# Performance work log

Hardware: AMD Instinct MI355X
Metric: run time of the kernel (lower is better)

Reference implementation:

```python
import jax, jax.numpy as jnp
import numpy as np

B, H, W, C = 64, 56, 56, 192
NH, WS, SS = 6, 7, 3
N = WS * WS
MLP_H = 4 * C
HD = C // NH
NW = (H // WS) * (W // WS)
EPS = 1e-5


def _rel_pos_index():
    coords = np.stack(np.meshgrid(np.arange(WS), np.arange(WS), indexing='ij')).reshape(2, -1)
    rel = (coords[:, :, None] - coords[:, None, :]).transpose(1, 2, 0)
    rel[..., 0] += WS - 1
    rel[..., 1] += WS - 1
    rel[..., 0] *= 2 * WS - 1
    return rel.sum(-1)  # [N, N]


def _attn_mask():
    img = np.zeros((H, W))
    cnt = 0
    sl = (slice(0, -WS), slice(-WS, -SS), slice(-SS, None))
    for hs in sl:
        for ws in sl:
            img[hs, ws] = cnt
            cnt += 1
    mw = img.reshape(H // WS, WS, W // WS, WS).transpose(0, 2, 1, 3).reshape(-1, N)
    am = mw[:, None, :] - mw[:, :, None]
    return np.where(am != 0, -100.0, 0.0).astype(np.float32)  # [nW, N, N]


REL_IDX = jnp.asarray(_rel_pos_index())
ATTN_MASK = jnp.asarray(_attn_mask())


def _ln(x, g, b):
    m = x.mean(-1, keepdims=True)
    v = x.var(-1, keepdims=True)
    return (x - m) / jnp.sqrt(v + EPS) * g + b


def setup_inputs() -> dict:
    key = jax.random.key(0)
    ks = jax.random.split(key, 16)
    p = lambda k, shape: jax.random.normal(k, shape, dtype=jnp.float32) * 0.02
    return {
        'x': jax.random.normal(ks[0], (B, H * W, C), dtype=jnp.float32),
        'norm1_g': jnp.ones((C,), jnp.float32),
        'norm1_b': jnp.zeros((C,), jnp.float32),
        'qkv_w': p(ks[1], (3 * C, C)),
        'qkv_b': jnp.zeros((3 * C,), jnp.float32),
        'rpb': p(ks[2], ((2 * WS - 1) * (2 * WS - 1), NH)),
        'gate': jnp.full((NH,), 0.001, jnp.float32),
        'proj_w': p(ks[3], (C, C)),
        'proj_b': jnp.zeros((C,), jnp.float32),
        'norm2_g': jnp.ones((C,), jnp.float32),
        'norm2_b': jnp.zeros((C,), jnp.float32),
        'fc1_w': p(ks[4], (MLP_H, C)),
        'fc1_b': jnp.zeros((MLP_H,), jnp.float32),
        'bn_g': jnp.ones((MLP_H,), jnp.float32),
        'bn_b': jnp.zeros((MLP_H,), jnp.float32),
        'fc2_w': p(ks[5], (C, MLP_H)),
        'fc2_b': jnp.zeros((C,), jnp.float32),
    }


def reference(x, norm1_g, norm1_b, qkv_w, qkv_b, rpb, gate, proj_w, proj_b,
              norm2_g, norm2_b, fc1_w, fc1_b, bn_g, bn_b, fc2_w, fc2_b):
    shortcut = x  # [B, L, C]
    y = _ln(x, norm1_g, norm1_b).reshape(B, H, W, C)
    # cyclic shift
    y = jnp.roll(y, (-SS, -SS), axis=(1, 2))
    # window partition -> [B*nW, N, C]
    yw = y.reshape(B, H // WS, WS, W // WS, WS, C).transpose(0, 1, 3, 2, 4, 5).reshape(-1, N, C)
    qkv = (yw @ qkv_w.T + qkv_b).reshape(-1, N, 3, NH, HD).transpose(2, 0, 3, 1, 4)
    q, k, v = qkv[0], qkv[1], qkv[2]  # [B_, NH, N, HD]
    scale = HD ** (-0.5)
    attn = jnp.einsum('bhnd,bhmd->bhnm', q * scale, k)  # [B_, NH, N, N]
    bias = rpb[REL_IDX].transpose(2, 0, 1)  # [NH, N, N]
    attn = attn + bias[None]
    attn = attn.reshape(B, NW, NH, N, N) + ATTN_MASK[None, :, None]
    attn = jax.nn.softmax(attn.reshape(-1, NH, N, N), axis=-1)
    attn = attn * jax.nn.sigmoid(gate).reshape(1, NH, 1, 1)  # post-softmax gate
    o = jnp.einsum('bhnm,bhmd->bhnd', attn, v).transpose(0, 2, 1, 3).reshape(-1, N, C)
    o = o @ proj_w.T + proj_b
    # window reverse + reverse shift
    o = o.reshape(B, H // WS, W // WS, WS, WS, C).transpose(0, 1, 3, 2, 4, 5).reshape(B, H, W, C)
    o = jnp.roll(o, (SS, SS), axis=(1, 2)).reshape(B, H * W, C)
    x = shortcut + o
    # MLP with eval-mode BatchNorm1d (running_mean=0, running_var=1)
    z = _ln(x, norm2_g, norm2_b)
    z = z @ fc1_w.T + fc1_b
    z = z / jnp.sqrt(1.0 + EPS) * bn_g + bn_b
    z = jax.nn.gelu(z, approximate=False)
    z = z @ fc2_w.T + fc2_b
    return x + z
```

## Files before the change

### kernel.cpp

```cpp
#include <hip/hip_runtime.h>
#include <hip/hip_bf16.h>
#include <math.h>


typedef __attribute__((ext_vector_type(8))) short short8;
typedef __attribute__((ext_vector_type(4))) short short4v;
typedef __attribute__((ext_vector_type(4))) float floatx4;

static __device__ __forceinline__ float bf2f(__hip_bfloat16 v) { return __bfloat162float(v); }

static __device__ __forceinline__ short f2bs(float f) {
    union { __hip_bfloat16 h; short s; } u;
    u.h = __float2bfloat16(f);
    return u.s;
}

__global__ __launch_bounds__(256)
void cvt_w(const float* __restrict__ a, const float* __restrict__ b,
           const float* __restrict__ c, const float* __restrict__ d,
           __hip_bfloat16* __restrict__ o)
{
    int i = blockIdx.x * 256 + threadIdx.x;
    float v;
    if (i < 110592)      v = a[i];
    else if (i < 147456) v = b[i - 110592];
    else if (i < 294912) {
        int l = i - 147456;
        int j = l & 7, ln = (l >> 3) & 63, t = l >> 9;
        int ks = t % 6, cc = t / 6;
        v = c[(cc * 16 + (ln & 15)) * 192 + ks * 32 + (ln >> 4) * 8 + j];
    } else {
        int l = i - 294912;
        int j = l & 7, ln = (l >> 3) & 63, t = l >> 9;
        int kg = t % 24, cc = t / 24;
        v = d[(cc * 16 + (ln & 15)) * 768 + kg * 32 + (ln >> 4) * 8 + j];
    }
    o[i] = __float2bfloat16(v);
}

__global__ __launch_bounds__(256)
void ln1_shift_win(const float* __restrict__ x,
                   const float* __restrict__ g,
                   const float* __restrict__ bt,
                   __hip_bfloat16* __restrict__ yw)
{
    int r = blockIdx.x * 4 + (threadIdx.x >> 6);
    int lane = threadIdx.x & 63;
    int win = r / 49, t = r - win * 49;
    int b = win >> 6, wi = win & 63;
    int wh = wi >> 3, ww = wi & 7;
    int tr = t / 7, tc = t - tr * 7;
    int hs = wh * 7 + tr + 3; if (hs >= 56) hs -= 56;
    int ws = ww * 7 + tc + 3; if (ws >= 56) ws -= 56;
    const float* src = x + ((size_t)b * 3136 + hs * 56 + ws) * 192;
    float v0 = src[lane];
    float v1 = src[lane + 64];
    float v2 = src[lane + 128];
    float s  = v0 + v1 + v2;
    float s2 = v0 * v0 + v1 * v1 + v2 * v2;
#pragma unroll
    for (int off = 32; off; off >>= 1) { s += __shfl_xor(s, off); s2 += __shfl_xor(s2, off); }
    float mean = s * (1.0f / 192.0f);
    float var  = s2 * (1.0f / 192.0f) - mean * mean;
    float rstd = rsqrtf(var + 1e-5f);
    __hip_bfloat16* dst = yw + (size_t)r * 192;
    dst[lane]       = __float2bfloat16((v0 - mean) * rstd * g[lane]       + bt[lane]);
    dst[lane + 64]  = __float2bfloat16((v1 - mean) * rstd * g[lane + 64]  + bt[lane + 64]);
    dst[lane + 128] = __float2bfloat16((v2 - mean) * rstd * g[lane + 128] + bt[lane + 128]);
}

__global__ __launch_bounds__(256)
void build_tbl(const float* __restrict__ rpb, float* __restrict__ tbl)
{
    int bid = blockIdx.x;
    int head = bid >> 2, cls = bid & 3;
    int ch = cls >> 1, cw = cls & 1;
    for (int idx = threadIdx.x; idx < 4096; idx += 256) {
        int tile = idx >> 8, lane = (idx >> 2) & 63, rg = idx & 3;
        int mt = tile >> 2, nt = tile & 3;
        int lm = lane & 15, quad = lane >> 4;
        int i = nt * 16 + lm;
        int j = mt * 16 + quad * 4 + rg;
        float v;
        if (i >= 49 || j >= 49) {
            v = -1e30f;
        } else {
            int ri = i / 7, ci = i - ri * 7;
            int rj = j / 7, cj = j - rj * 7;
            int bidx = (ri - rj + 6) * 13 + (ci - cj + 6);
            v = rpb[bidx * 6 + head];
            int rio = ch ? (ri < 4 ? 1 : 2) : 0;
            int cio = cw ? (ci < 4 ? 1 : 2) : 0;
            int rjo = ch ? (rj < 4 ? 1 : 2) : 0;
            int cjo = cw ? (cj < 4 ? 1 : 2) : 0;
            if (rio * 3 + cio != rjo * 3 + cjo) v -= 100.0f;
        }
        tbl[(size_t)bid * 4096 + idx] = v;
    }
}

__global__ __launch_bounds__(256)
void attn_mfma(const __hip_bfloat16* __restrict__ qkv,
               const float* __restrict__ tbl,
               const float* __restrict__ gate,
               __hip_bfloat16* __restrict__ o)
{
    __shared__ __align__(16) char lds[49152];
    const int wave = threadIdx.x >> 6, lane = threadIdx.x & 63;
    const int lm = lane & 15, quad = lane >> 4;
    const int idx = blockIdx.x * 4 + wave;
    const int win = idx / 6;
    const int head = idx - win * 6;
    const int wi = win & 63;
    const int cls = (((wi >> 3) == 7) ? 2 : 0) + (((wi & 7) == 7) ? 1 : 0);

    char* vTb = lds + wave * 12288;
    char* Pb  = vTb + 4096;

    const __hip_bfloat16* base = qkv + (size_t)win * 49 * 576 + head * 32;

    {
        short8 v0 = {0,0,0,0,0,0,0,0}, v1 = {0,0,0,0,0,0,0,0};
        short8 v2 = {0,0,0,0,0,0,0,0}, v3 = {0,0,0,0,0,0,0,0};
        if (lane < 49) {
            const short* p = (const short*)(base + 384) + (size_t)lane * 576;
            v0 = *(const short8*)(p);
            v1 = *(const short8*)(p + 8);
            v2 = *(const short8*)(p + 16);
            v3 = *(const short8*)(p + 24);
        }
#pragma unroll
        for (int d = 0; d < 32; ++d) {
            short val = (d < 8) ? v0[d & 7] : (d < 16) ? v1[d & 7] : (d < 24) ? v2[d & 7] : v3[d & 7];
            *(short*)(vTb + ((d * 128 + lane * 2) ^ ((d & 7) << 4))) = val;
        }
    }

    short8 qf[4], kf[4];
    const short* qsrc = (const short*)base + quad * 8;
    const short* ksrc = (const short*)(base + 192) + quad * 8;
#pragma unroll
    for (int tt = 0; tt < 4; ++tt) {
        int t = tt * 16 + lm;
        if (t < 49) {
            qf[tt] = *(const short8*)(qsrc + (size_t)t * 576);
            kf[tt] = *(const short8*)(ksrc + (size_t)t * 576);
        } else {
            qf[tt] = (short8){0,0,0,0,0,0,0,0};
            kf[tt] = (short8){0,0,0,0,0,0,0,0};
        }
    }

    const floatx4 z4 = {0.f, 0.f, 0.f, 0.f};
    floatx4 s[4][4];
#pragma unroll
    for (int mt = 0; mt < 4; ++mt)
#pragma unroll
        for (int nt = 0; nt < 4; ++nt)
            s[mt][nt] = __builtin_amdgcn_mfma_f32_16x16x32_bf16(kf[mt], qf[nt], z4, 0, 0, 0);

    const float* tb = tbl + (size_t)(head * 4 + cls) * 4096 + lane * 4;
#pragma unroll
    for (int mt = 0; mt < 4; ++mt)
#pragma unroll
        for (int nt = 0; nt < 4; ++nt) {
            floatx4 b = *(const floatx4*)(tb + (mt * 4 + nt) * 256);
#pragma unroll
            for (int rg = 0; rg < 4; ++rg)
                s[mt][nt][rg] = s[mt][nt][rg] * 0.17677669529663689f + b[rg];
        }

    const float gt = 1.0f / (1.0f + __expf(-gate[head]));

    float inv[4];
#pragma unroll
    for (int nt = 0; nt < 4; ++nt) {
        float mx = -1e30f;
#pragma unroll
        for (int mt = 0; mt < 4; ++mt)
#pragma unroll
            for (int rg = 0; rg < 4; ++rg) mx = fmaxf(mx, s[mt][nt][rg]);
        mx = fmaxf(mx, __shfl_xor(mx, 16));
        mx = fmaxf(mx, __shfl_xor(mx, 32));
        float sum = 0.f;
#pragma unroll
        for (int mt = 0; mt < 4; ++mt)
#pragma unroll
            for (int rg = 0; rg < 4; ++rg) {
                float e = __expf(s[mt][nt][rg] - mx);
                s[mt][nt][rg] = e;
                sum += e;
            }
        sum += __shfl_xor(sum, 16);
        sum += __shfl_xor(sum, 32);
        inv[nt] = gt / sum;
    }

#pragma unroll
    for (int nt = 0; nt < 4; ++nt) {
        int row = nt * 16 + lm;
#pragma unroll
        for (int mt = 0; mt < 4; ++mt) {
            short4v pk = { f2bs(s[mt][nt][0] * inv[nt]), f2bs(s[mt][nt][1] * inv[nt]),
                           f2bs(s[mt][nt][2] * inv[nt]), f2bs(s[mt][nt][3] * inv[nt]) };
            int off = (row * 128 + mt * 32 + quad * 8) ^ ((row & 7) << 4);
            *(short4v*)(Pb + off) = pk;
        }
    }

    floatx4 oacc[4][2];
#pragma unroll
    for (int pt = 0; pt < 4; ++pt)
#pragma unroll
        for (int nt = 0; nt < 2; ++nt) oacc[pt][nt] = z4;

#pragma unroll
    for (int ks = 0; ks < 2; ++ks) {
        short8 vfr[2];
#pragma unroll
        for (int nt = 0; nt < 2; ++nt) {
            int row = nt * 16 + lm;
            vfr[nt] = *(const short8*)(vTb + ((row * 128 + ks * 64 + quad * 16) ^ ((row & 7) << 4)));
        }
#pragma unroll
        for (int pt = 0; pt < 4; ++pt) {
            int row = pt * 16 + lm;
            short8 pfr = *(const short8*)(Pb + ((row * 128 + ks * 64 + quad * 16) ^ ((row & 7) << 4)));
#pragma unroll
            for (int nt = 0; nt < 2; ++nt)
                oacc[pt][nt] = __builtin_amdgcn_mfma_f32_16x16x32_bf16(pfr, vfr[nt], oacc[pt][nt], 0, 0, 0);
        }
    }

    __hip_bfloat16* obase = o + (size_t)win * 49 * 192 + head * 32;
#pragma unroll
    for (int pt = 0; pt < 4; ++pt) {
#pragma unroll
        for (int rg = 0; rg < 4; ++rg) {
            int q = pt * 16 + quad * 4 + rg;
            if (q < 49) {
#pragma unroll
                for (int nt = 0; nt < 2; ++nt)
                    obase[(size_t)q * 192 + nt * 16 + lm] = __float2bfloat16(oacc[pt][nt][rg]);
            }
        }
    }
}

template <int MODE>
__global__ __launch_bounds__(256, 2)
void gemm_bt(const __hip_bfloat16* __restrict__ A,
             const __hip_bfloat16* __restrict__ W,
             const float* __restrict__ bias,
             const float* __restrict__ ex0,
             void* __restrict__ OutV,
             int K, int Ncols)
{
    __shared__ __align__(16) char lds[(128 * 32 + 64 * 32) * 2];
    short* sA = (short*)lds;
    short* sB = (short*)(lds + 8192);

    const int tid  = threadIdx.x;
    const int wave = tid >> 6, lane = tid & 63;
    const int m0 = blockIdx.x * 128;
    const int n0 = blockIdx.y * 64;
    const int wm = wave >> 1, wn = wave & 1;
    const int lm = lane & 15, quad = lane >> 4;

    floatx4 acc[4][2];
#pragma unroll
    for (int mt = 0; mt < 4; ++mt)
#pragma unroll
        for (int nt = 0; nt < 2; ++nt) acc[mt][nt] = (floatx4){0.f, 0.f, 0.f, 0.f};

    for (int kk = 0; kk < K; kk += 32) {
#pragma unroll
        for (int i = 0; i < 2; ++i) {
            int c = i * 256 + tid;
            int row = c >> 2, kc = c & 3;
            const __hip_bfloat16* gp = A + (size_t)(m0 + row) * K + kk + kc * 8;
            char* lp = lds + (i * 256 + wave * 64) * 16;
            __builtin_amdgcn_global_load_lds((const __attribute__((address_space(1))) void*)gp,
                                             (__attribute__((address_space(3))) void*)lp, 16, 0, 0);
        }
        {
            int c = tid;
            int row = c >> 2, kc = c & 3;
            const __hip_bfloat16* gp = W + (size_t)(n0 + row) * K + kk + kc * 8;
            char* lp = lds + 8192 + (wave * 64) * 16;
            __builtin_amdgcn_global_load_lds((const __attribute__((address_space(1))) void*)gp,
                                             (__attribute__((address_space(3))) void*)lp, 16, 0, 0);
        }
        asm volatile("s_waitcnt vmcnt(0)" ::: "memory");
        __syncthreads();

        short8 af[4], bf[2];
#pragma unroll
        for (int mt = 0; mt < 4; ++mt)
            af[mt] = *(const short8*)(sA + ((wm * 64 + mt * 16 + lm) * 32 + quad * 8));
#pragma unroll
        for (int nt = 0; nt < 2; ++nt)
            bf[nt] = *(const short8*)(sB + ((wn * 32 + nt * 16 + lm) * 32 + quad * 8));
#pragma unroll
        for (int mt = 0; mt < 4; ++mt)
#pragma unroll
            for (int nt = 0; nt < 2; ++nt)
                acc[mt][nt] = __builtin_amdgcn_mfma_f32_16x16x32_bf16(af[mt], bf[nt], acc[mt][nt], 0, 0, 0);
        __syncthreads();
    }

#pragma unroll
    for (int mt = 0; mt < 4; ++mt) {
#pragma unroll
        for (int nt = 0; nt < 2; ++nt) {
            int col = n0 + wn * 32 + nt * 16 + lm;
            float bcol = bias[col];
#pragma unroll
            for (int rg = 0; rg < 4; ++rg) {
                int row = m0 + wm * 64 + mt * 16 + quad * 4 + rg;
                float val = acc[mt][nt][rg] + bcol;
                if (MODE == 0) {
                    ((__hip_bfloat16*)OutV)[(size_t)row * Ncols + col] = __float2bfloat16(val);
                } else {
                    int win = row / 49, t = row - win * 49;
                    int b = win >> 6, wi = win & 63;
                    int wh = wi >> 3, ww = wi & 7;
                    int tr = t / 7, tc = t - tr * 7;
                    int h = wh * 7 + tr + 3; if (h >= 56) h -= 56;
                    int w = ww * 7 + tc + 3; if (w >= 56) w -= 56;
                    size_t dst = ((size_t)b * 3136 + h * 56 + w) * 192 + col;
                    ((float*)OutV)[dst] = val + ex0[dst];
                }
            }
        }
    }
}

__global__ __launch_bounds__(256, 2)
void mlp_fused(float* __restrict__ xio,
               const __hip_bfloat16* __restrict__ w1f,
               const __hip_bfloat16* __restrict__ w2f,
               const float* __restrict__ fc1_b,
               const float* __restrict__ bn_g,
               const float* __restrict__ bn_b,
               const float* __restrict__ fc2_b,
               const float* __restrict__ n2g,
               const float* __restrict__ n2b)
{
    __shared__ __align__(16) char zb[128 * 384];
    __shared__ __align__(16) char hbf[128 * 128];

    const int tid = threadIdx.x;
    const int wave = tid >> 6, lane = tid & 63;
    const int lm = lane & 15, quad = lane >> 4;
    const int wm = wave >> 1, wn = wave & 1;
    const int m0 = blockIdx.x * 128;

    {
        float g0 = n2g[lane], g1 = n2g[lane + 64], g2 = n2g[lane + 128];
        float b0 = n2b[lane], b1 = n2b[lane + 64], b2 = n2b[lane + 128];
        for (int rr = 0; rr < 32; ++rr) {
            int row = wave * 32 + rr;
            const float* src = xio + (size_t)(m0 + row) * 192;
            float v0 = src[lane], v1 = src[lane + 64], v2 = src[lane + 128];
            float s = v0 + v1 + v2;
            float s2 = v0 * v0 + v1 * v1 + v2 * v2;
#pragma unroll
            for (int off = 32; off; off >>= 1) { s += __shfl_xor(s, off); s2 += __shfl_xor(s2, off); }
            float mean = s * (1.0f / 192.0f);
            float var  = s2 * (1.0f / 192.0f) - mean * mean;
            float rstd = rsqrtf(var + 1e-5f);
            int rx = (row & 7) << 4;
            int rb = row * 384;
            *(short*)(zb + ((rb + lane * 2)       ^ rx)) = f2bs((v0 - mean) * rstd * g0 + b0);
            *(short*)(zb + ((rb + 128 + lane * 2) ^ rx)) = f2bs((v1 - mean) * rstd * g1 + b1);
            *(short*)(zb + ((rb + 256 + lane * 2) ^ rx)) = f2bs((v2 - mean) * rstd * g2 + b2);
        }
    }
    __syncthreads();

    floatx4 acc[4][6];
#pragma unroll
    for (int mt = 0; mt < 4; ++mt)
#pragma unroll
        for (int nt = 0; nt < 6; ++nt) acc[mt][nt] = (floatx4){0.f, 0.f, 0.f, 0.f};

    const short8* w1v = (const short8*)w1f;
    const short8* w2v = (const short8*)w2f;

    for (int s = 0; s < 12; ++s) {
        {
            floatx4 a2[4][2];
#pragma unroll
            for (int mt = 0; mt < 4; ++mt)
#pragma unroll
                for (int nt = 0; nt < 2; ++nt) a2[mt][nt] = (floatx4){0.f, 0.f, 0.f, 0.f};
            const int c0 = s * 4 + wn * 2;
#pragma unroll
            for (int ks = 0; ks < 6; ++ks) {
                short8 wf0 = w1v[(size_t)(c0 * 6 + ks) * 64 + lane];
                short8 wf1 = w1v[(size_t)((c0 + 1) * 6 + ks) * 64 + lane];
                short8 zf[4];
#pragma unroll
                for (int mt = 0; mt < 4; ++mt) {
                    int row = wm * 64 + mt * 16 + lm;
                    int byte = (row * 384 + ks * 64 + quad * 16) ^ ((row & 7) << 4);
                    zf[mt] = *(const short8*)(zb + byte);
                }
#pragma unroll
                for (int mt = 0; mt < 4; ++mt) {
                    a2[mt][0] = __builtin_amdgcn_mfma_f32_16x16x32_bf16(wf0, zf[mt], a2[mt][0], 0, 0, 0);
                    a2[mt][1] = __builtin_amdgcn_mfma_f32_16x16x32_bf16(wf1, zf[mt], a2[mt][1], 0, 0, 0);
                }
            }
#pragma unroll
            for (int nt = 0; nt < 2; ++nt) {
                int colb = (c0 + nt) * 16 + quad * 4;
                float fb[4], G[4], B2[4];
#pragma unroll
                for (int rg = 0; rg < 4; ++rg) {
                    fb[rg] = fc1_b[colb + rg];
                    G[rg]  = bn_g[colb + rg] * 0.99999500003749968f;
                    B2[rg] = bn_b[colb + rg];
                }
#pragma unroll
                for (int mt = 0; mt < 4; ++mt) {
                    int row = wm * 64 + mt * 16 + lm;
                    short4v pk;
#pragma unroll
                    for (int rg = 0; rg < 4; ++rg) {
                        float t2 = (a2[mt][nt][rg] + fb[rg]) * G[rg] + B2[rg];
                        float ge = 0.5f * t2 * (1.0f + erff(t2 * 0.70710678118654752f));
                        pk[rg] = f2bs(ge);
                    }
                    int byte = (row * 128 + (wn * 2 + nt) * 32 + quad * 8) ^ ((row & 7) << 4);
                    *(short4v*)(hbf + byte) = pk;
                }
            }
        }
        __syncthreads();
        {
#pragma unroll
            for (int ks = 0; ks < 2; ++ks) {
                const int kg = s * 2 + ks;
                short8 vf[6];
#pragma unroll
                for (int nt = 0; nt < 6; ++nt)
                    vf[nt] = w2v[(size_t)((wn * 6 + nt) * 24 + kg) * 64 + lane];
                short8 hf[4];
#pragma unroll
                for (int mt = 0; mt < 4; ++mt) {
                    int row = wm * 64 + mt * 16 + lm;
                    int byte = (row * 128 + ks * 64 + quad * 16) ^ ((row & 7) << 4);
                    hf[mt] = *(const short8*)(hbf + byte);
                }
#pragma unroll
                for (int mt = 0; mt < 4; ++mt)
#pragma unroll
                    for (int nt = 0; nt < 6; ++nt)
                        acc[mt][nt] = __builtin_amdgcn_mfma_f32_16x16x32_bf16(hf[mt], vf[nt], acc[mt][nt], 0, 0, 0);
            }
        }
        __syncthreads();
    }

#pragma unroll
    for (int nt = 0; nt < 6; ++nt) {
        int col = wn * 96 + nt * 16 + lm;
        float fb = fc2_b[col];
#pragma unroll
        for (int mt = 0; mt < 4; ++mt) {
#pragma unroll
            for (int rg = 0; rg < 4; ++rg) {
                size_t dst = (size_t)(m0 + wm * 64 + mt * 16 + quad * 4 + rg) * 192 + col;
                xio[dst] = acc[mt][nt][rg] + fb + xio[dst];
            }
        }
    }
}

extern "C" void kernel_launch(void* const* d_in, const int* in_sizes, int n_in,
                              void* d_out, int out_size, void* d_ws, size_t ws_size,
                              hipStream_t stream)
{
    const float* x      = (const float*)d_in[0];
    const float* n1g    = (const float*)d_in[1];
    const float* n1b    = (const float*)d_in[2];
    const float* qkv_w  = (const float*)d_in[3];
    const float* qkv_b  = (const float*)d_in[4];
    const float* rpb    = (const float*)d_in[5];
    const float* gate   = (const float*)d_in[6];
    const float* proj_w = (const float*)d_in[7];
    const float* proj_b = (const float*)d_in[8];
    const float* n2g    = (const float*)d_in[9];
    const float* n2b    = (const float*)d_in[10];
    const float* fc1_w  = (const float*)d_in[11];
    const float* fc1_b  = (const float*)d_in[12];
    const float* bn_g   = (const float*)d_in[13];
    const float* bn_b   = (const float*)d_in[14];
    const float* fc2_w  = (const float*)d_in[15];
    const float* fc2_b  = (const float*)d_in[16];
    float* out = (float*)d_out;

    char* ws = (char*)d_ws;
    const int NCH = (ws_size >= 155025408u) ? 4 : 8;
    const size_t buf1max = (NCH == 4) ? 77070336u : 38535168u;
    __hip_bfloat16* buf0 = (__hip_bfloat16*)(ws);
    __hip_bfloat16* buf1 = (__hip_bfloat16*)(ws + 77070336);
    __hip_bfloat16* wbuf = (__hip_bfloat16*)(ws + 77070336 + buf1max);
    __hip_bfloat16* wq  = wbuf;
    __hip_bfloat16* wp  = wbuf + 110592;
    __hip_bfloat16* w1f = wbuf + 147456;
    __hip_bfloat16* w2f = wbuf + 294912;

    const int WINS = 4096 / NCH;
    const int ROWS = WINS * 49;
    const int GX   = ROWS / 128;

    float* tbl = (float*)(ws + 77070336 + (size_t)ROWS * 576 * 2);

    cvt_w<<<dim3(1728), 256, 0, stream>>>(qkv_w, proj_w, fc1_w, fc2_w, wbuf);
    build_tbl<<<dim3(24), 256, 0, stream>>>(rpb, tbl);

    ln1_shift_win<<<dim3(200704 / 4), 256, 0, stream>>>(x, n1g, n1b, buf0);

    for (int c = 0; c < NCH; ++c) {
        const __hip_bfloat16* ywc = buf0 + (size_t)c * ROWS * 192;
        __hip_bfloat16*       oc  = buf0 + (size_t)c * ROWS * 192;
        gemm_bt<0><<<dim3(GX, 9), 256, 0, stream>>>(ywc, wq, qkv_b, nullptr, buf1, 192, 576);
        attn_mfma<<<dim3(WINS * 6 / 4), 256, 0, stream>>>(buf1, tbl, gate, oc);
    }

    gemm_bt<1><<<dim3(1568, 3), 256, 0, stream>>>(buf0, wp, proj_b, x, out, 192, 192);

    mlp_fused<<<dim3(1568), 256, 0, stream>>>(out, w1f, w2f, fc1_b, bn_g, bn_b, fc2_b, n2g, n2b);
}
```

Measured before the change: 972.2 us.

## Restructure fused MLP: register-resident activations, LDS double-buffered weights via direct loads

Rewrites the fused MLP kernel so each wave owns 32 token rows. The LayerNorm output is kept in registers as MFMA fragments, and the GELU hidden tile is passed to the second GEMM through cross-lane shuffles instead of round-tripping through shared memory. Weights for both GEMMs are streamed per 32-column hidden chunk into a double-buffered LDS region using global_load_lds, with the fc2 weight prepack reordered to match. This removes the LDS activation staging and one barrier per step and overlaps weight fetch with compute. The cost is more accumulator registers per wave (24 tiles), which may lower occupancy.

```diff
diff --git a/kernel.cpp b/kernel.cpp
--- a/kernel.cpp
+++ b/kernel.cpp
@@ -32,8 +32,8 @@
     } else {
         int l = i - 294912;
         int j = l & 7, ln = (l >> 3) & 63, t = l >> 9;
-        int kg = t % 24, cc = t / 24;
-        v = d[(cc * 16 + (ln & 15)) * 768 + kg * 32 + (ln >> 4) * 8 + j];
+        int ct = t % 12, kg = t / 12;
+        v = d[(ct * 16 + (ln & 15)) * 768 + kg * 32 + (ln >> 4) * 8 + j];
     }
     o[i] = __float2bfloat16(v);
 }
@@ -347,133 +347,163 @@
                const float* __restrict__ n2g,
                const float* __restrict__ n2b)
 {
-    __shared__ __align__(16) char zb[128 * 384];
-    __shared__ __align__(16) char hbf[128 * 128];
+    __shared__ __align__(16) char wlds[2][24576];
 
     const int tid = threadIdx.x;
     const int wave = tid >> 6, lane = tid & 63;
     const int lm = lane & 15, quad = lane >> 4;
-    const int wm = wave >> 1, wn = wave & 1;
-    const int m0 = blockIdx.x * 128;
-
+    const int t0 = blockIdx.x * 128 + wave * 32;
+
+    short8 zf[2][6];
     {
-        float g0 = n2g[lane], g1 = n2g[lane + 64], g2 = n2g[lane + 128];
-        float b0 = n2b[lane], b1 = n2b[lane + 64], b2 = n2b[lane + 128];
-        for (int rr = 0; rr < 32; ++rr) {
-            int row = wave * 32 + rr;
-            const float* src = xio + (size_t)(m0 + row) * 192;
-            float v0 = src[lane], v1 = src[lane + 64], v2 = src[lane + 128];
-            float s = v0 + v1 + v2;
-            float s2 = v0 * v0 + v1 * v1 + v2 * v2;
-#pragma unroll
-            for (int off = 32; off; off >>= 1) { s += __shfl_xor(s, off); s2 += __shfl_xor(s2, off); }
+        floatx4 gg[6][2], bb[6][2];
+#pragma unroll
+        for (int ks = 0; ks < 6; ++ks) {
+            gg[ks][0] = *(const floatx4*)(n2g + ks * 32 + quad * 8);
+            gg[ks][1] = *(const floatx4*)(n2g + ks * 32 + quad * 8 + 4);
+            bb[ks][0] = *(const floatx4*)(n2b + ks * 32 + quad * 8);
+            bb[ks][1] = *(const floatx4*)(n2b + ks * 32 + quad * 8 + 4);
+        }
+#pragma unroll
+        for (int mt = 0; mt < 2; ++mt) {
+            const float* src = xio + (size_t)(t0 + mt * 16 + lm) * 192 + quad * 8;
+            floatx4 v[6][2];
+#pragma unroll
+            for (int ks = 0; ks < 6; ++ks) {
+                v[ks][0] = *(const floatx4*)(src + ks * 32);
+                v[ks][1] = *(const floatx4*)(src + ks * 32 + 4);
+            }
+            float s = 0.f, s2 = 0.f;
+#pragma unroll
+            for (int ks = 0; ks < 6; ++ks)
+#pragma unroll
+                for (int h = 0; h < 2; ++h)
+#pragma unroll
+                    for (int r = 0; r < 4; ++r) { float x = v[ks][h][r]; s += x; s2 += x * x; }
+            s  += __shfl_xor(s, 16);  s  += __shfl_xor(s, 32);
+            s2 += __shfl_xor(s2, 16); s2 += __shfl_xor(s2, 32);
             float mean = s * (1.0f / 192.0f);
             float var  = s2 * (1.0f / 192.0f) - mean * mean;
             float rstd = rsqrtf(var + 1e-5f);
-            int rx = (row & 7) << 4;
-            int rb = row * 384;
-            *(short*)(zb + ((rb + lane * 2)       ^ rx)) = f2bs((v0 - mean) * rstd * g0 + b0);
-            *(short*)(zb + ((rb + 128 + lane * 2) ^ rx)) = f2bs((v1 - mean) * rstd * g1 + b1);
-            *(short*)(zb + ((rb + 256 + lane * 2) ^ rx)) = f2bs((v2 - mean) * rstd * g2 + b2);
-        }
-    }
+#pragma unroll
+            for (int ks = 0; ks < 6; ++ks)
+#pragma unroll
+                for (int h = 0; h < 2; ++h)
+#pragma unroll
+                    for (int r = 0; r < 4; ++r) {
+                        float nv = (v[ks][h][r] - mean) * rstd * gg[ks][h][r] + bb[ks][h][r];
+                        zf[mt][ks][h * 4 + r] = f2bs(nv);
+                    }
+        }
+    }
+
+    floatx4 acc[2][12];
+#pragma unroll
+    for (int mt = 0; mt < 2; ++mt)
+#pragma unroll
+        for (int ct = 0; ct < 12; ++ct) acc[mt][ct] = (floatx4){0.f, 0.f, 0.f, 0.f};
+
+    auto stage = [&](int kg, int p) {
+        const char* g1 = (const char*)w1f + (size_t)kg * 12288 + wave * 1024 + lane * 16;
+        const char* g2 = (const char*)w2f + (size_t)kg * 12288 + wave * 1024 + lane * 16;
+        char* l1 = &wlds[p][0] + wave * 1024;
+        char* l2 = &wlds[p][0] + 12288 + wave * 1024;
+#pragma unroll
+        for (int i = 0; i < 3; ++i) {
+            __builtin_amdgcn_global_load_lds((const __attribute__((address_space(1))) void*)(g1 + i * 4096),
+                                             (__attribute__((address_space(3))) void*)(l1 + i * 4096), 16, 0, 0);
+            __builtin_amdgcn_global_load_lds((const __attribute__((address_space(1))) void*)(g2 + i * 4096),
+                                             (__attribute__((address_space(3))) void*)(l2 + i * 4096), 16, 0, 0);
+        }
+    };
+
+    stage(0, 0);
+    asm volatile("s_waitcnt vmcnt(0)" ::: "memory");
     __syncthreads();
 
-    floatx4 acc[4][6];
-#pragma unroll
-    for (int mt = 0; mt < 4; ++mt)
-#pragma unroll
-        for (int nt = 0; nt < 6; ++nt) acc[mt][nt] = (floatx4){0.f, 0.f, 0.f, 0.f};
-
-    const short8* w1v = (const short8*)w1f;
-    const short8* w2v = (const short8*)w2f;
-
-    for (int s = 0; s < 12; ++s) {
-        {
-            floatx4 a2[4][2];
-#pragma unroll
-            for (int mt = 0; mt < 4; ++mt)
-#pragma unroll
-                for (int nt = 0; nt < 2; ++nt) a2[mt][nt] = (floatx4){0.f, 0.f, 0.f, 0.f};
-            const int c0 = s * 4 + wn * 2;
-#pragma unroll
-            for (int ks = 0; ks < 6; ++ks) {
-                short8 wf0 = w1v[(size_t)(c0 * 6 + ks) * 64 + lane];
-                short8 wf1 = w1v[(size_t)((c0 + 1) * 6 + ks) * 64 + lane];
-                short8 zf[4];
-#pragma unroll
-                for (int mt = 0; mt < 4; ++mt) {
-                    int row = wm * 64 + mt * 16 + lm;
-                    int byte = (row * 384 + ks * 64 + quad * 16) ^ ((row & 7) << 4);
-                    zf[mt] = *(const short8*)(zb + byte);
+    const int srcA = (quad & 1) * 32 + lm;
+    const int srcB = srcA + 16;
+    const int hi = quad >> 1;
+
+    int cur = 0;
+    for (int kg = 0; kg < 24; ++kg) {
+        if (kg < 23) stage(kg + 1, cur ^ 1);
+        const char* sw1 = &wlds[cur][0];
+        const char* sw2 = &wlds[cur][0] + 12288;
+
+        floatx4 aa[2][2];
+#pragma unroll
+        for (int mt = 0; mt < 2; ++mt)
+#pragma unroll
+            for (int u = 0; u < 2; ++u) aa[mt][u] = (floatx4){0.f, 0.f, 0.f, 0.f};
+#pragma unroll
+        for (int ks = 0; ks < 6; ++ks) {
+            short8 wf0 = *(const short8*)(sw1 + ks * 1024 + lane * 16);
+            short8 wf1 = *(const short8*)(sw1 + 6144 + ks * 1024 + lane * 16);
+#pragma unroll
+            for (int mt = 0; mt < 2; ++mt) {
+                aa[mt][0] = __builtin_amdgcn_mfma_f32_16x16x32_bf16(wf0, zf[mt][ks], aa[mt][0], 0, 0, 0);
+                aa[mt][1] = __builtin_amdgcn_mfma_f32_16x16x32_bf16(wf1, zf[mt][ks], aa[mt][1], 0, 0, 0);
+            }
+        }
+
+        int pw[2][2][2];
+#pragma unroll
+        for (int u = 0; u < 2; ++u) {
+            int colb = kg * 32 + u * 16 + quad * 4;
+            floatx4 fb = *(const floatx4*)(fc1_b + colb);
+            floatx4 G  = *(const floatx4*)(bn_g + colb);
+            floatx4 Bb = *(const floatx4*)(bn_b + colb);
+#pragma unroll
+            for (int mt = 0; mt < 2; ++mt) {
+                short hs[4];
+#pragma unroll
+                for (int rg = 0; rg < 4; ++rg) {
+                    float t2 = (aa[mt][u][rg] + fb[rg]) * (G[rg] * 0.99999500003749968f) + Bb[rg];
+                    float ge = 0.5f * t2 * (1.0f + erff(t2 * 0.70710678118654752f));
+                    hs[rg] = f2bs(ge);
                 }
-#pragma unroll
-                for (int mt = 0; mt < 4; ++mt) {
-                    a2[mt][0] = __builtin_amdgcn_mfma_f32_16x16x32_bf16(wf0, zf[mt], a2[mt][0], 0, 0, 0);
-                    a2[mt][1] = __builtin_amdgcn_mfma_f32_16x16x32_bf16(wf1, zf[mt], a2[mt][1], 0, 0, 0);
-                }
-            }
-#pragma unroll
-            for (int nt = 0; nt < 2; ++nt) {
-                int colb = (c0 + nt) * 16 + quad * 4;
-                float fb[4], G[4], B2[4];
-#pragma unroll
-                for (int rg = 0; rg < 4; ++rg) {
-                    fb[rg] = fc1_b[colb + rg];
-                    G[rg]  = bn_g[colb + rg] * 0.99999500003749968f;
-                    B2[rg] = bn_b[colb + rg];
-                }
-#pragma unroll
-                for (int mt = 0; mt < 4; ++mt) {
-                    int row = wm * 64 + mt * 16 + lm;
-                    short4v pk;
-#pragma unroll
-                    for (int rg = 0; rg < 4; ++rg) {
-                        float t2 = (a2[mt][nt][rg] + fb[rg]) * G[rg] + B2[rg];
-                        float ge = 0.5f * t2 * (1.0f + erff(t2 * 0.70710678118654752f));
-                        pk[rg] = f2bs(ge);
-                    }
-                    int byte = (row * 128 + (wn * 2 + nt) * 32 + quad * 8) ^ ((row & 7) << 4);
-                    *(short4v*)(hbf + byte) = pk;
-                }
-            }
-        }
+                pw[mt][u][0] = (int)(unsigned short)hs[0] | ((int)(unsigned short)hs[1] << 16);
+                pw[mt][u][1] = (int)(unsigned short)hs[2] | ((int)(unsigned short)hs[3] << 16);
+            }
+        }
+
+        short8 hf[2];
+#pragma unroll
+        for (int mt = 0; mt < 2; ++mt) {
+            int a0 = __shfl(pw[mt][0][0], srcA), a1 = __shfl(pw[mt][0][1], srcA);
+            int a2 = __shfl(pw[mt][0][0], srcB), a3 = __shfl(pw[mt][0][1], srcB);
+            int b0 = __shfl(pw[mt][1][0], srcA), b1 = __shfl(pw[mt][1][1], srcA);
+            int b2 = __shfl(pw[mt][1][0], srcB), b3 = __shfl(pw[mt][1][1], srcB);
+            union { int i[4]; short8 s; } u4;
+            u4.i[0] = hi ? b0 : a0;
+            u4.i[1] = hi ? b1 : a1;
+            u4.i[2] = hi ? b2 : a2;
+            u4.i[3] = hi ? b3 : a3;
+            hf[mt] = u4.s;
+        }
+
+#pragma unroll 4
+        for (int ct = 0; ct < 12; ++ct) {
+            short8 vf = *(const short8*)(sw2 + ct * 1024 + lane * 16);
+            acc[0][ct] = __builtin_amdgcn_mfma_f32_16x16x32_bf16(hf[0], vf, acc[0][ct], 0, 0, 0);
+            acc[1][ct] = __builtin_amdgcn_mfma_f32_16x16x32_bf16(hf[1], vf, acc[1][ct], 0, 0, 0);
+        }
+
+        asm volatile("s_waitcnt vmcnt(0)" ::: "memory");
         __syncthreads();
-        {
-#pragma unroll
-            for (int ks = 0; ks < 2; ++ks) {
-                const int kg = s * 2 + ks;
-                short8 vf[6];
-#pragma unroll
-                for (int nt = 0; nt < 6; ++nt)
-                    vf[nt] = w2v[(size_t)((wn * 6 + nt) * 24 + kg) * 64 + lane];
-                short8 hf[4];
-#pragma unroll
-                for (int mt = 0; mt < 4; ++mt) {
-                    int row = wm * 64 + mt * 16 + lm;
-                    int byte = (row * 128 + ks * 64 + quad * 16) ^ ((row & 7) << 4);
-                    hf[mt] = *(const short8*)(hbf + byte);
-                }
-#pragma unroll
-                for (int mt = 0; mt < 4; ++mt)
-#pragma unroll
-                    for (int nt = 0; nt < 6; ++nt)
-                        acc[mt][nt] = __builtin_amdgcn_mfma_f32_16x16x32_bf16(hf[mt], vf[nt], acc[mt][nt], 0, 0, 0);
-            }
-        }
-        __syncthreads();
-    }
-
-#pragma unroll
-    for (int nt = 0; nt < 6; ++nt) {
-        int col = wn * 96 + nt * 16 + lm;
-        float fb = fc2_b[col];
-#pragma unroll
-        for (int mt = 0; mt < 4; ++mt) {
+        cur ^= 1;
+    }
+
+#pragma unroll
+    for (int ct = 0; ct < 12; ++ct) {
+        float fb = fc2_b[ct * 16 + lm];
+#pragma unroll
+        for (int mt = 0; mt < 2; ++mt) {
 #pragma unroll
             for (int rg = 0; rg < 4; ++rg) {
-                size_t dst = (size_t)(m0 + wm * 64 + mt * 16 + quad * 4 + rg) * 192 + col;
-                xio[dst] = acc[mt][nt][rg] + fb + xio[dst];
+                size_t dst = (size_t)(t0 + mt * 16 + quad * 4 + rg) * 192 + ct * 16 + lm;
+                xio[dst] = acc[mt][ct][rg] + fb + xio[dst];
             }
         }
     }
```

New measurement: 1.870 ms. +92.3%, slower.
